# Kernel tuning notes

Measured on AMD Instinct MI355X. Metric: run time of the kernel, lower is better.

Reference implementation:

```python
import jax, jax.numpy as jnp
import numpy as np

N = 100000      # nodes
E = 1600000     # edges (avg degree 16)
D_IN, D_H, D_OUT = 128, 128, 64
NORM_SCALE = 1.0
EPS = 1e-6


def setup_inputs() -> dict:
    key = jax.random.key(0)
    ks = jax.random.split(key, 9)
    x = jax.random.normal(ks[0], (N, D_IN), dtype=jnp.float32)
    edge_index = jax.random.randint(ks[1], (2, E), 0, N, dtype=jnp.int32)
    edge_weight = jax.random.uniform(ks[2], (E,), dtype=jnp.float32)
    # GraphConv = Linear then spmm(adj, .); Glorot-ish init for weights
    W0 = jax.random.normal(ks[3], (D_IN, D_H), dtype=jnp.float32) / np.float32(np.sqrt(D_IN))
    b0 = jnp.zeros((D_H,), jnp.float32)
    W1 = jax.random.normal(ks[4], (D_H, D_H), dtype=jnp.float32) / np.float32(np.sqrt(D_H))
    b1 = jnp.zeros((D_H,), jnp.float32)
    Wout = jax.random.normal(ks[5], (D_H, D_OUT), dtype=jnp.float32) / np.float32(np.sqrt(D_H))
    bout = jnp.zeros((D_OUT,), jnp.float32)
    return {"x": x, "edge_index": edge_index, "edge_weight": edge_weight,
            "W0": W0, "b0": b0, "W1": W1, "b1": b1, "Wout": Wout, "bout": bout}


def _pair_norm(h):
    # PairNorm mode 'PN': center columns, divide by sqrt(mean squared row norm)
    h = h - jnp.mean(h, axis=0, keepdims=True)
    rownorm_mean = jnp.sqrt(EPS + jnp.mean(jnp.sum(h * h, axis=1)))
    return NORM_SCALE * h / rownorm_mean


def reference(x, edge_index, edge_weight, W0, b0, W1, b1, Wout, bout):
    src = edge_index[0]
    dst = edge_index[1]

    def graph_conv(h, W, b):
        h = h @ W + b                              # [N, d_out]
        msg = edge_weight[:, None] * h[src]        # [E, d_out] gather
        return jax.ops.segment_sum(msg, dst, num_segments=N)  # spmm(adj, h)

    x_old = jnp.zeros((), jnp.float32)
    for (W, b) in ((W0, b0), (W1, b1)):
        # dropout p=0 -> identity (omitted)
        h = graph_conv(x, W, b)
        h = jax.nn.relu(_pair_norm(h))
        x = h + x_old        # residual=1 -> skip every layer
        x_old = x
    return graph_conv(x, Wout, bout)
```

## Files before the change

kernel.cpp:

```cpp
#include <hip/hip_runtime.h>

#define N_NODES 100000
#define N_EDGES 1600000
#define DH 128
#define DOUT 64
#define EPS 1e-6f
#define NBINS 8
#define BINW 12500
#define NREP 64

typedef __attribute__((ext_vector_type(8))) short s8v;
typedef __attribute__((ext_vector_type(4))) float f32x4;

__device__ inline unsigned bfround(float f) {
    unsigned u = __float_as_uint(f);
    return (u + 0x7fffu + ((u >> 16) & 1u)) >> 16;
}
__device__ inline unsigned pack2(float a, float b) { return bfround(a) | (bfround(b) << 16); }
__device__ inline float blo(unsigned u) { return __uint_as_float(u << 16); }
__device__ inline float bhi(unsigned u) { return __uint_as_float(u & 0xffff0000u); }

template <int COLS, int PN>
__global__ __launch_bounds__(256) void gemm_mfma(const void* __restrict__ Xav,
                                                 const float* __restrict__ muA,
                                                 const float* __restrict__ invA,
                                                 const unsigned* __restrict__ Xbu2,
                                                 const float* __restrict__ muB,
                                                 const float* __restrict__ invB,
                                                 const float* __restrict__ W,
                                                 const float* __restrict__ bias,
                                                 unsigned* __restrict__ Y, int nrows) {
    constexpr int CT = COLS / 16;
    __shared__ unsigned wtu[COLS][64];
    __shared__ unsigned xbu[64][64];

    const int tid = threadIdx.x;
    const int wv = tid >> 6;
    const int lane = tid & 63;
    const float sA = (PN >= 1) ? invA[0] : 0.f;
    const float sB = (PN == 2) ? invB[0] : 0.f;

    {
        ushort* wts = (ushort*)wtu;
        constexpr int NV4 = 128 * COLS / 4;
        for (int i = tid; i < NV4; i += 256) {
            int k = i / (COLS / 4);
            int c4 = i % (COLS / 4);
            float4 w4 = reinterpret_cast<const float4*>(W)[i];
            float vals[4] = {w4.x, w4.y, w4.z, w4.w};
            int u = k >> 1, kb = k & 1;
#pragma unroll
            for (int j = 0; j < 4; ++j) {
                int c = c4 * 4 + j;
                int us = u ^ ((c & 7) << 2);
                wts[c * 128 + us * 2 + kb] = (ushort)bfround(vals[j]);
            }
        }
    }

    float bv[CT];
#pragma unroll
    for (int f = 0; f < CT; ++f) bv[f] = bias[f * 16 + (lane & 15)];

    const int row0 = blockIdx.x * 128;
    const int myr = (wv << 4) + (lane & 15);

#pragma unroll
    for (int ms = 0; ms < 2; ++ms) {
        const int rb = row0 + ms * 64;
        __syncthreads();
        if constexpr (PN == 0) {
            const float* Xa = (const float*)Xav;
            for (int i = tid; i < 2048; i += 256) {
                int r = i >> 5;
                int c4 = i & 31;
                float4 v = make_float4(0.f, 0.f, 0.f, 0.f);
                if (rb + r < nrows) v = reinterpret_cast<const float4*>(Xa + (size_t)(rb + r) * 128)[c4];
                int sw = (r & 7) << 2;
                xbu[r][(c4 * 2) ^ sw] = pack2(v.x, v.y);
                xbu[r][(c4 * 2 + 1) ^ sw] = pack2(v.z, v.w);
            }
        } else {
            const unsigned* Xa = (const unsigned*)Xav;
            for (int i = tid; i < 1024; i += 256) {
                int r = i >> 4;
                int c4 = i & 15;
                float v0 = 0.f, v1 = 0.f, v2 = 0.f, v3 = 0.f, v4 = 0.f, v5 = 0.f, v6 = 0.f,
                      v7 = 0.f;
                if (rb + r < nrows) {
                    uint4 uv = reinterpret_cast<const uint4*>(Xa + (size_t)(rb + r) * 64)[c4];
                    float4 ma = reinterpret_cast<const float4*>(muA)[c4 * 2];
                    float4 mb = reinterpret_cast<const float4*>(muA)[c4 * 2 + 1];
                    v0 = fmaxf((blo(uv.x) - ma.x) * sA, 0.f);
                    v1 = fmaxf((bhi(uv.x) - ma.y) * sA, 0.f);
                    v2 = fmaxf((blo(uv.y) - ma.z) * sA, 0.f);
                    v3 = fmaxf((bhi(uv.y) - ma.w) * sA, 0.f);
                    v4 = fmaxf((blo(uv.z) - mb.x) * sA, 0.f);
                    v5 = fmaxf((bhi(uv.z) - mb.y) * sA, 0.f);
                    v6 = fmaxf((blo(uv.w) - mb.z) * sA, 0.f);
                    v7 = fmaxf((bhi(uv.w) - mb.w) * sA, 0.f);
                    if constexpr (PN == 2) {
                        uint4 u2 = reinterpret_cast<const uint4*>(Xbu2 + (size_t)(rb + r) * 64)[c4];
                        float4 na = reinterpret_cast<const float4*>(muB)[c4 * 2];
                        float4 nb = reinterpret_cast<const float4*>(muB)[c4 * 2 + 1];
                        v0 += fmaxf((blo(u2.x) - na.x) * sB, 0.f);
                        v1 += fmaxf((bhi(u2.x) - na.y) * sB, 0.f);
                        v2 += fmaxf((blo(u2.y) - na.z) * sB, 0.f);
                        v3 += fmaxf((bhi(u2.y) - na.w) * sB, 0.f);
                        v4 += fmaxf((blo(u2.z) - nb.x) * sB, 0.f);
                        v5 += fmaxf((bhi(u2.z) - nb.y) * sB, 0.f);
                        v6 += fmaxf((blo(u2.w) - nb.z) * sB, 0.f);
                        v7 += fmaxf((bhi(u2.w) - nb.w) * sB, 0.f);
                    }
                }
                int sw = (r & 7) << 2;
                xbu[r][(c4 * 4 + 0) ^ sw] = pack2(v0, v1);
                xbu[r][(c4 * 4 + 1) ^ sw] = pack2(v2, v3);
                xbu[r][(c4 * 4 + 2) ^ sw] = pack2(v4, v5);
                xbu[r][(c4 * 4 + 3) ^ sw] = pack2(v6, v7);
            }
        }
        __syncthreads();

        f32x4 acc[CT];
#pragma unroll
        for (int f = 0; f < CT; ++f) acc[f] = (f32x4){0.f, 0.f, 0.f, 0.f};
        const int xsw = (myr & 7) << 2;
#pragma unroll
        for (int kc = 0; kc < 4; ++kc) {
            const int u0 = kc * 16 + (lane >> 4) * 4;
            s8v a = *reinterpret_cast<const s8v*>(&xbu[myr][u0 ^ xsw]);
#pragma unroll
            for (int f = 0; f < CT; ++f) {
                const int c = f * 16 + (lane & 15);
                s8v b = *reinterpret_cast<const s8v*>(&wtu[c][u0 ^ ((c & 7) << 2)]);
                acc[f] = __builtin_amdgcn_mfma_f32_16x16x32_bf16(a, b, acc[f], 0, 0, 0);
            }
        }

#pragma unroll
        for (int f = 0; f < CT; ++f) {
#pragma unroll
            for (int r = 0; r < 4; ++r) {
                float v = acc[f][r] + bv[f];
                float p = __shfl_xor(v, 1, 64);
                unsigned pk = (lane & 1) ? pack2(p, v) : pack2(v, p);
                int grow = rb + (wv << 4) + ((lane >> 4) << 2) + r;
                if (grow < nrows && ((lane & 1) == (f & 1))) {
                    Y[(size_t)grow * (COLS / 2) + f * 8 + ((lane & 15) >> 1)] = pk;
                }
            }
        }
    }
}

__global__ __launch_bounds__(256) void hist_kernel(const int* __restrict__ dst,
                                                   int* __restrict__ counts) {
    int i = blockIdx.x * blockDim.x + threadIdx.x;
    const int stride = gridDim.x * blockDim.x;
    for (; i < N_EDGES / 4; i += stride) {
        int4 d = reinterpret_cast<const int4*>(dst)[i];
        atomicAdd(&counts[d.x], 1);
        atomicAdd(&counts[d.y], 1);
        atomicAdd(&counts[d.z], 1);
        atomicAdd(&counts[d.w], 1);
    }
}

__global__ __launch_bounds__(1024) void scan_kernel(const int* __restrict__ counts,
                                                    int* __restrict__ rowptr) {
    __shared__ int wsum[16];
    const int tid = threadIdx.x;
    const int lane = tid & 63;
    const int w = tid >> 6;
    int offset = 0;
    if (tid == 0) rowptr[0] = 0;
    for (int base = 0; base < N_NODES; base += 4096) {
        int i = base + tid * 4;
        int4 v = make_int4(0, 0, 0, 0);
        if (i < N_NODES) v = *reinterpret_cast<const int4*>(counts + i);
        int p0 = v.x, p1 = p0 + v.y, p2 = p1 + v.z, p3 = p2 + v.w;
        int incl = p3;
#pragma unroll
        for (int d = 1; d < 64; d <<= 1) {
            int t = __shfl_up(incl, d, 64);
            if (lane >= d) incl += t;
        }
        if (lane == 63) wsum[w] = incl;
        __syncthreads();
        if (w == 0 && lane < 16) {
            int t = wsum[lane];
#pragma unroll
            for (int d = 1; d < 16; d <<= 1) {
                int u = __shfl_up(t, d, 64);
                if (lane >= d) t += u;
            }
            wsum[lane] = t;
        }
        __syncthreads();
        int woff = (w == 0) ? 0 : wsum[w - 1];
        int chunk_total = wsum[15];
        int tbase = offset + woff + incl - p3;
        if (i < N_NODES) {
            rowptr[i + 1] = tbase + p0;
            rowptr[i + 2] = tbase + p1;
            rowptr[i + 3] = tbase + p2;
            rowptr[i + 4] = tbase + p3;
        }
        offset += chunk_total;
        __syncthreads();
    }
}

__global__ __launch_bounds__(256) void bucket_kernel(const int* __restrict__ src,
                                                     const int* __restrict__ dst,
                                                     const float* __restrict__ ew,
                                                     const int* __restrict__ rowptr,
                                                     int* __restrict__ fill,
                                                     int2* __restrict__ em) {
    const int myBin = blockIdx.x & (NBINS - 1);
    const int lo = myBin * BINW;
    const int hi = lo + BINW;
    int e = (blockIdx.x >> 3) * 256 + threadIdx.x;
    const int stride = (gridDim.x >> 3) * 256;
    for (; e < N_EDGES; e += stride) {
        int d = dst[e];
        if (d >= lo && d < hi) {
            int pos = atomicAdd(&fill[d], 1);
            em[rowptr[d] + pos] = make_int2(src[e], __float_as_int(ew[e]));
        }
    }
}

__global__ __launch_bounds__(256) void agg128b_kernel(const unsigned* __restrict__ Hb,
                                                      const int* __restrict__ rowptr,
                                                      const int2* __restrict__ em,
                                                      unsigned* __restrict__ Bb,
                                                      float* __restrict__ cs_part,
                                                      float* __restrict__ ss_part) {
    __shared__ int2 smeta[4][64];
    __shared__ float cs[4][128];
    __shared__ float ssw[4];
    const int wv = threadIdx.x >> 6;
    const int lane = threadIdx.x & 63;
    const int half = lane >> 5;
    const int col2 = lane & 31;
    const int node = blockIdx.x * 4 + wv;
    const int beg = rowptr[node];
    const int end = rowptr[node + 1];
    const int2* sm = smeta[wv];
    float a0 = 0.f, a1 = 0.f, a2 = 0.f, a3 = 0.f;

    for (int c = beg; c < end; c += 64) {
        smeta[wv][lane] = (c + lane < end) ? em[c + lane] : make_int2(0, 0);
        const int cnt = min(64, end - c);
        const int rounds = (cnt + 15) >> 4;
        for (int g = 0; g < rounds; ++g) {
            const int b = g * 16 + half;
            int2 m0 = sm[b + 0];
            int2 m1 = sm[b + 2];
            int2 m2 = sm[b + 4];
            int2 m3 = sm[b + 6];
            int2 m4 = sm[b + 8];
            int2 m5 = sm[b + 10];
            int2 m6 = sm[b + 12];
            int2 m7 = sm[b + 14];
            uint2 u0 = *reinterpret_cast<const uint2*>(Hb + (size_t)m0.x * 64 + col2 * 2);
            uint2 u1 = *reinterpret_cast<const uint2*>(Hb + (size_t)m1.x * 64 + col2 * 2);
            uint2 u2 = *reinterpret_cast<const uint2*>(Hb + (size_t)m2.x * 64 + col2 * 2);
            uint2 u3 = *reinterpret_cast<const uint2*>(Hb + (size_t)m3.x * 64 + col2 * 2);
            uint2 u4 = *reinterpret_cast<const uint2*>(Hb + (size_t)m4.x * 64 + col2 * 2);
            uint2 u5 = *reinterpret_cast<const uint2*>(Hb + (size_t)m5.x * 64 + col2 * 2);
            uint2 u6 = *reinterpret_cast<const uint2*>(Hb + (size_t)m6.x * 64 + col2 * 2);
            uint2 u7 = *reinterpret_cast<const uint2*>(Hb + (size_t)m7.x * 64 + col2 * 2);
            float w0 = __int_as_float(m0.y), w1 = __int_as_float(m1.y);
            float w2 = __int_as_float(m2.y), w3 = __int_as_float(m3.y);
            float w4 = __int_as_float(m4.y), w5 = __int_as_float(m5.y);
            float w6 = __int_as_float(m6.y), w7 = __int_as_float(m7.y);
            a0 += w0 * blo(u0.x); a1 += w0 * bhi(u0.x); a2 += w0 * blo(u0.y); a3 += w0 * bhi(u0.y);
            a0 += w1 * blo(u1.x); a1 += w1 * bhi(u1.x); a2 += w1 * blo(u1.y); a3 += w1 * bhi(u1.y);
            a0 += w2 * blo(u2.x); a1 += w2 * bhi(u2.x); a2 += w2 * blo(u2.y); a3 += w2 * bhi(u2.y);
            a0 += w3 * blo(u3.x); a1 += w3 * bhi(u3.x); a2 += w3 * blo(u3.y); a3 += w3 * bhi(u3.y);
            a0 += w4 * blo(u4.x); a1 += w4 * bhi(u4.x); a2 += w4 * blo(u4.y); a3 += w4 * bhi(u4.y);
            a0 += w5 * blo(u5.x); a1 += w5 * bhi(u5.x); a2 += w5 * blo(u5.y); a3 += w5 * bhi(u5.y);
            a0 += w6 * blo(u6.x); a1 += w6 * bhi(u6.x); a2 += w6 * blo(u6.y); a3 += w6 * bhi(u6.y);
            a0 += w7 * blo(u7.x); a1 += w7 * bhi(u7.x); a2 += w7 * blo(u7.y); a3 += w7 * bhi(u7.y);
        }
    }
    a0 += __shfl_xor(a0, 32, 64);
    a1 += __shfl_xor(a1, 32, 64);
    a2 += __shfl_xor(a2, 32, 64);
    a3 += __shfl_xor(a3, 32, 64);

    float sq = 0.f;
    if (lane < 32) {
        uint2 op;
        op.x = pack2(a0, a1);
        op.y = pack2(a2, a3);
        *reinterpret_cast<uint2*>(Bb + (size_t)node * 64 + col2 * 2) = op;
        cs[wv][col2 * 4 + 0] = a0;
        cs[wv][col2 * 4 + 1] = a1;
        cs[wv][col2 * 4 + 2] = a2;
        cs[wv][col2 * 4 + 3] = a3;
        sq = a0 * a0 + a1 * a1 + a2 * a2 + a3 * a3;
    }
#pragma unroll
    for (int off = 32; off; off >>= 1) sq += __shfl_down(sq, off, 64);
    if (lane == 0) ssw[wv] = sq;
    __syncthreads();
    const int rep = blockIdx.x & (NREP - 1);
    if (threadIdx.x < 128) {
        float s = cs[0][threadIdx.x] + cs[1][threadIdx.x] + cs[2][threadIdx.x] + cs[3][threadIdx.x];
        atomicAdd(&cs_part[rep * 128 + threadIdx.x], s);
    }
    if (threadIdx.x == 0) atomicAdd(&ss_part[rep], ssw[0] + ssw[1] + ssw[2] + ssw[3]);
}

__global__ __launch_bounds__(256) void agg64b_kernel(const unsigned* __restrict__ Hb,
                                                     const int* __restrict__ rowptr,
                                                     const int2* __restrict__ em,
                                                     float* __restrict__ out) {
    __shared__ int2 smeta[4][64];
    const int wv = threadIdx.x >> 6;
    const int lane = threadIdx.x & 63;
    const int q = lane >> 4;
    const int col2 = lane & 15;
    const int node = blockIdx.x * 4 + wv;
    const int beg = rowptr[node];
    const int end = rowptr[node + 1];
    const int2* sm = smeta[wv];
    float a0 = 0.f, a1 = 0.f, a2 = 0.f, a3 = 0.f;

    for (int c = beg; c < end; c += 64) {
        smeta[wv][lane] = (c + lane < end) ? em[c + lane] : make_int2(0, 0);
        const int cnt = min(64, end - c);
        const int rounds = (cnt + 31) >> 5;
        for (int g = 0; g < rounds; ++g) {
            const int b = g * 32 + q;
            int2 m0 = sm[b + 0];
            int2 m1 = sm[b + 4];
            int2 m2 = sm[b + 8];
            int2 m3 = sm[b + 12];
            int2 m4 = sm[b + 16];
            int2 m5 = sm[b + 20];
            int2 m6 = sm[b + 24];
            int2 m7 = sm[b + 28];
            uint2 u0 = *reinterpret_cast<const uint2*>(Hb + (size_t)m0.x * 32 + col2 * 2);
            uint2 u1 = *reinterpret_cast<const uint2*>(Hb + (size_t)m1.x * 32 + col2 * 2);
            uint2 u2 = *reinterpret_cast<const uint2*>(Hb + (size_t)m2.x * 32 + col2 * 2);
            uint2 u3 = *reinterpret_cast<const uint2*>(Hb + (size_t)m3.x * 32 + col2 * 2);
            uint2 u4 = *reinterpret_cast<const uint2*>(Hb + (size_t)m4.x * 32 + col2 * 2);
            uint2 u5 = *reinterpret_cast<const uint2*>(Hb + (size_t)m5.x * 32 + col2 * 2);
            uint2 u6 = *reinterpret_cast<const uint2*>(Hb + (size_t)m6.x * 32 + col2 * 2);
            uint2 u7 = *reinterpret_cast<const uint2*>(Hb + (size_t)m7.x * 32 + col2 * 2);
            float w0 = __int_as_float(m0.y), w1 = __int_as_float(m1.y);
            float w2 = __int_as_float(m2.y), w3 = __int_as_float(m3.y);
            float w4 = __int_as_float(m4.y), w5 = __int_as_float(m5.y);
            float w6 = __int_as_float(m6.y), w7 = __int_as_float(m7.y);
            a0 += w0 * blo(u0.x); a1 += w0 * bhi(u0.x); a2 += w0 * blo(u0.y); a3 += w0 * bhi(u0.y);
            a0 += w1 * blo(u1.x); a1 += w1 * bhi(u1.x); a2 += w1 * blo(u1.y); a3 += w1 * bhi(u1.y);
            a0 += w2 * blo(u2.x); a1 += w2 * bhi(u2.x); a2 += w2 * blo(u2.y); a3 += w2 * bhi(u2.y);
            a0 += w3 * blo(u3.x); a1 += w3 * bhi(u3.x); a2 += w3 * blo(u3.y); a3 += w3 * bhi(u3.y);
            a0 += w4 * blo(u4.x); a1 += w4 * bhi(u4.x); a2 += w4 * blo(u4.y); a3 += w4 * bhi(u4.y);
            a0 += w5 * blo(u5.x); a1 += w5 * bhi(u5.x); a2 += w5 * blo(u5.y); a3 += w5 * bhi(u5.y);
            a0 += w6 * blo(u6.x); a1 += w6 * bhi(u6.x); a2 += w6 * blo(u6.y); a3 += w6 * bhi(u6.y);
            a0 += w7 * blo(u7.x); a1 += w7 * bhi(u7.x); a2 += w7 * blo(u7.y); a3 += w7 * bhi(u7.y);
        }
    }
    a0 += __shfl_xor(a0, 16, 64); a0 += __shfl_xor(a0, 32, 64);
    a1 += __shfl_xor(a1, 16, 64); a1 += __shfl_xor(a1, 32, 64);
    a2 += __shfl_xor(a2, 16, 64); a2 += __shfl_xor(a2, 32, 64);
    a3 += __shfl_xor(a3, 16, 64); a3 += __shfl_xor(a3, 32, 64);
    if (lane < 16) {
        *reinterpret_cast<float4*>(out + (size_t)node * DOUT + col2 * 4) =
            make_float4(a0, a1, a2, a3);
    }
}

__global__ void finalize_stats(const float* __restrict__ cs_part,
                               const float* __restrict__ ss_part, float* __restrict__ mu,
                               float* __restrict__ inv) {
    const int t = threadIdx.x;
    float m = 0.f;
    for (int r = 0; r < NREP; ++r) m += cs_part[r * 128 + t];
    float mean = m / (float)N_NODES;
    mu[t] = mean;
    float v = mean * mean;
    __shared__ float partl[2];
    __shared__ float sstot;
#pragma unroll
    for (int off = 32; off; off >>= 1) v += __shfl_down(v, off, 64);
    if ((t & 63) == 0) partl[t >> 6] = v;
    float ss = (t < NREP) ? ss_part[t] : 0.f;
#pragma unroll
    for (int off = 32; off; off >>= 1) ss += __shfl_down(ss, off, 64);
    if (t == 0) sstot = ss;
    __syncthreads();
    if (t == 0) {
        float musq = partl[0] + partl[1];
        float s = (sstot - (float)N_NODES * musq) / (float)N_NODES;
        inv[0] = rsqrtf(EPS + s);
    }
}

extern "C" void kernel_launch(void* const* d_in, const int* in_sizes, int n_in,
                              void* d_out, int out_size, void* d_ws, size_t ws_size,
                              hipStream_t stream) {
    const float* x = (const float*)d_in[0];
    const int* edge_index = (const int*)d_in[1];
    const float* ew = (const float*)d_in[2];
    const float* W0 = (const float*)d_in[3];
    const float* b0 = (const float*)d_in[4];
    const float* W1 = (const float*)d_in[5];
    const float* b1 = (const float*)d_in[6];
    const float* Wout = (const float*)d_in[7];
    const float* bout = (const float*)d_in[8];

    const int* src = edge_index;
    const int* dst = edge_index + N_EDGES;
    float* out = (float*)d_out;

    unsigned* base = (unsigned*)d_ws;
    unsigned* Hb = base;
    unsigned* B1b = base + (size_t)N_NODES * 64;
    unsigned* B2b = B1b + (size_t)N_NODES * 64;
    int2* em = (int2*)(B2b + (size_t)N_NODES * 64);
    int* counts = (int*)(em + N_EDGES);
    int* fill = counts + N_NODES;
    int* rowptr = fill + N_NODES;
    size_t soff = (size_t)(rowptr + N_NODES + 1 - (int*)base);
    soff = (soff + 3) & ~(size_t)3;
    float* stats = (float*)base + soff;
    float* cs_part1 = stats;
    float* ss_part1 = cs_part1 + NREP * 128;
    float* cs_part2 = ss_part1 + NREP;
    float* ss_part2 = cs_part2 + NREP * 128;
    float* mu1 = ss_part2 + NREP;
    float* inv1 = mu1 + 128;
    float* mu2 = inv1 + 4;
    float* inv2 = mu2 + 128;

    const int gemm_grid = (N_NODES + 127) / 128;
    const int agg_grid = N_NODES / 4;

    hipMemsetAsync(counts, 0, (size_t)2 * N_NODES * sizeof(int), stream);
    hipMemsetAsync(stats, 0, (size_t)2 * (NREP * 128 + NREP) * sizeof(float), stream);

    hist_kernel<<<1024, 256, 0, stream>>>(dst, counts);
    scan_kernel<<<1, 1024, 0, stream>>>(counts, rowptr);
    bucket_kernel<<<2048, 256, 0, stream>>>(src, dst, ew, rowptr, fill, em);

    gemm_mfma<128, 0><<<gemm_grid, 256, 0, stream>>>(
        x, nullptr, nullptr, nullptr, nullptr, nullptr, W0, b0, Hb, N_NODES);
    agg128b_kernel<<<agg_grid, 256, 0, stream>>>(Hb, rowptr, em, B1b, cs_part1, ss_part1);
    finalize_stats<<<1, 128, 0, stream>>>(cs_part1, ss_part1, mu1, inv1);

    gemm_mfma<128, 1><<<gemm_grid, 256, 0, stream>>>(
        B1b, mu1, inv1, nullptr, nullptr, nullptr, W1, b1, Hb, N_NODES);
    agg128b_kernel<<<agg_grid, 256, 0, stream>>>(Hb, rowptr, em, B2b, cs_part2, ss_part2);
    finalize_stats<<<1, 128, 0, stream>>>(cs_part2, ss_part2, mu2, inv2);

    gemm_mfma<64, 2><<<gemm_grid, 256, 0, stream>>>(
        B2b, mu2, inv2, B1b, mu1, inv1, Wout, bout, Hb, N_NODES);
    agg64b_kernel<<<agg_grid, 256, 0, stream>>>(Hb, rowptr, em, out);
}
```

Baseline: 539.4 us.

## Split 128-wide aggregation into column slices across blocks for cache locality

Replaces the per-node full-row aggregation kernel with a column-sliced version. Each block handles one of eight 16-column slices for 16 nodes, and each wave processes 16 edges at a time with 4 lanes per edge. The aim is a smaller working set per concurrent block slice, so gathered rows hit in cache better and more gathers are in flight per wave. In exchange, the edge metadata (em, rowptr) is re-read eight times, each gather is only 16 bytes, and there are more shuffle reductions and atomics.

```diff
diff --git a/kernel.cpp b/kernel.cpp
--- a/kernel.cpp
+++ b/kernel.cpp
@@ -232,88 +232,71 @@
     }
 }
 
-__global__ __launch_bounds__(256) void agg128b_kernel(const unsigned* __restrict__ Hb,
+__global__ __launch_bounds__(256) void agg128s_kernel(const unsigned* __restrict__ Hb,
                                                       const int* __restrict__ rowptr,
                                                       const int2* __restrict__ em,
                                                       unsigned* __restrict__ Bb,
                                                       float* __restrict__ cs_part,
                                                       float* __restrict__ ss_part) {
-    __shared__ int2 smeta[4][64];
-    __shared__ float cs[4][128];
-    __shared__ float ssw[4];
+    const int slice = blockIdx.x & 7;
+    const int grp = blockIdx.x >> 3;
     const int wv = threadIdx.x >> 6;
     const int lane = threadIdx.x & 63;
-    const int half = lane >> 5;
-    const int col2 = lane & 31;
-    const int node = blockIdx.x * 4 + wv;
-    const int beg = rowptr[node];
-    const int end = rowptr[node + 1];
-    const int2* sm = smeta[wv];
-    float a0 = 0.f, a1 = 0.f, a2 = 0.f, a3 = 0.f;
-
-    for (int c = beg; c < end; c += 64) {
-        smeta[wv][lane] = (c + lane < end) ? em[c + lane] : make_int2(0, 0);
-        const int cnt = min(64, end - c);
-        const int rounds = (cnt + 15) >> 4;
-        for (int g = 0; g < rounds; ++g) {
-            const int b = g * 16 + half;
-            int2 m0 = sm[b + 0];
-            int2 m1 = sm[b + 2];
-            int2 m2 = sm[b + 4];
-            int2 m3 = sm[b + 6];
-            int2 m4 = sm[b + 8];
-            int2 m5 = sm[b + 10];
-            int2 m6 = sm[b + 12];
-            int2 m7 = sm[b + 14];
-            uint2 u0 = *reinterpret_cast<const uint2*>(Hb + (size_t)m0.x * 64 + col2 * 2);
-            uint2 u1 = *reinterpret_cast<const uint2*>(Hb + (size_t)m1.x * 64 + col2 * 2);
-            uint2 u2 = *reinterpret_cast<const uint2*>(Hb + (size_t)m2.x * 64 + col2 * 2);
-            uint2 u3 = *reinterpret_cast<const uint2*>(Hb + (size_t)m3.x * 64 + col2 * 2);
-            uint2 u4 = *reinterpret_cast<const uint2*>(Hb + (size_t)m4.x * 64 + col2 * 2);
-            uint2 u5 = *reinterpret_cast<const uint2*>(Hb + (size_t)m5.x * 64 + col2 * 2);
-            uint2 u6 = *reinterpret_cast<const uint2*>(Hb + (size_t)m6.x * 64 + col2 * 2);
-            uint2 u7 = *reinterpret_cast<const uint2*>(Hb + (size_t)m7.x * 64 + col2 * 2);
-            float w0 = __int_as_float(m0.y), w1 = __int_as_float(m1.y);
-            float w2 = __int_as_float(m2.y), w3 = __int_as_float(m3.y);
-            float w4 = __int_as_float(m4.y), w5 = __int_as_float(m5.y);
-            float w6 = __int_as_float(m6.y), w7 = __int_as_float(m7.y);
-            a0 += w0 * blo(u0.x); a1 += w0 * bhi(u0.x); a2 += w0 * blo(u0.y); a3 += w0 * bhi(u0.y);
-            a0 += w1 * blo(u1.x); a1 += w1 * bhi(u1.x); a2 += w1 * blo(u1.y); a3 += w1 * bhi(u1.y);
-            a0 += w2 * blo(u2.x); a1 += w2 * bhi(u2.x); a2 += w2 * blo(u2.y); a3 += w2 * bhi(u2.y);
-            a0 += w3 * blo(u3.x); a1 += w3 * bhi(u3.x); a2 += w3 * blo(u3.y); a3 += w3 * bhi(u3.y);
-            a0 += w4 * blo(u4.x); a1 += w4 * bhi(u4.x); a2 += w4 * blo(u4.y); a3 += w4 * bhi(u4.y);
-            a0 += w5 * blo(u5.x); a1 += w5 * bhi(u5.x); a2 += w5 * blo(u5.y); a3 += w5 * bhi(u5.y);
-            a0 += w6 * blo(u6.x); a1 += w6 * bhi(u6.x); a2 += w6 * blo(u6.y); a3 += w6 * bhi(u6.y);
-            a0 += w7 * blo(u7.x); a1 += w7 * bhi(u7.x); a2 += w7 * blo(u7.y); a3 += w7 * bhi(u7.y);
-        }
-    }
-    a0 += __shfl_xor(a0, 32, 64);
-    a1 += __shfl_xor(a1, 32, 64);
-    a2 += __shfl_xor(a2, 32, 64);
-    a3 += __shfl_xor(a3, 32, 64);
-
-    float sq = 0.f;
-    if (lane < 32) {
-        uint2 op;
-        op.x = pack2(a0, a1);
-        op.y = pack2(a2, a3);
-        *reinterpret_cast<uint2*>(Bb + (size_t)node * 64 + col2 * 2) = op;
-        cs[wv][col2 * 4 + 0] = a0;
-        cs[wv][col2 * 4 + 1] = a1;
-        cs[wv][col2 * 4 + 2] = a2;
-        cs[wv][col2 * 4 + 3] = a3;
-        sq = a0 * a0 + a1 * a1 + a2 * a2 + a3 * a3;
-    }
-#pragma unroll
-    for (int off = 32; off; off >>= 1) sq += __shfl_down(sq, off, 64);
-    if (lane == 0) ssw[wv] = sq;
-    __syncthreads();
-    const int rep = blockIdx.x & (NREP - 1);
-    if (threadIdx.x < 128) {
-        float s = cs[0][threadIdx.x] + cs[1][threadIdx.x] + cs[2][threadIdx.x] + cs[3][threadIdx.x];
-        atomicAdd(&cs_part[rep * 128 + threadIdx.x], s);
-    }
-    if (threadIdx.x == 0) atomicAdd(&ss_part[rep], ssw[0] + ssw[1] + ssw[2] + ssw[3]);
+    const int sub = lane >> 2;
+    const int f = lane & 3;
+    const unsigned* hsl = Hb + slice * 8 + f * 2;
+    const int nbase = grp * 16 + wv * 4;
+
+    float cs0 = 0.f, cs1 = 0.f, cs2 = 0.f, cs3 = 0.f, ssl = 0.f;
+
+#pragma unroll
+    for (int nn = 0; nn < 4; ++nn) {
+        const int node = nbase + nn;
+        const int beg = rowptr[node];
+        const int end = rowptr[node + 1];
+        float a0 = 0.f, a1 = 0.f, a2 = 0.f, a3 = 0.f;
+        for (int c = beg; c < end; c += 16) {
+            const int ei = c + sub;
+            int2 m = (ei < end) ? em[ei] : make_int2(0, 0);
+            uint2 u = *reinterpret_cast<const uint2*>(hsl + (size_t)m.x * 64);
+            float w = __int_as_float(m.y);
+            a0 += w * blo(u.x);
+            a1 += w * bhi(u.x);
+            a2 += w * blo(u.y);
+            a3 += w * bhi(u.y);
+        }
+        a0 += __shfl_xor(a0, 4, 64); a0 += __shfl_xor(a0, 8, 64);
+        a0 += __shfl_xor(a0, 16, 64); a0 += __shfl_xor(a0, 32, 64);
+        a1 += __shfl_xor(a1, 4, 64); a1 += __shfl_xor(a1, 8, 64);
+        a1 += __shfl_xor(a1, 16, 64); a1 += __shfl_xor(a1, 32, 64);
+        a2 += __shfl_xor(a2, 4, 64); a2 += __shfl_xor(a2, 8, 64);
+        a2 += __shfl_xor(a2, 16, 64); a2 += __shfl_xor(a2, 32, 64);
+        a3 += __shfl_xor(a3, 4, 64); a3 += __shfl_xor(a3, 8, 64);
+        a3 += __shfl_xor(a3, 16, 64); a3 += __shfl_xor(a3, 32, 64);
+        if (lane < 4) {
+            uint2 op;
+            op.x = pack2(a0, a1);
+            op.y = pack2(a2, a3);
+            *reinterpret_cast<uint2*>(Bb + (size_t)node * 64 + slice * 8 + lane * 2) = op;
+            cs0 += a0;
+            cs1 += a1;
+            cs2 += a2;
+            cs3 += a3;
+            ssl += a0 * a0 + a1 * a1 + a2 * a2 + a3 * a3;
+        }
+    }
+
+    const int rep = grp & (NREP - 1);
+    if (lane < 4) {
+        float* cp = &cs_part[rep * 128 + slice * 16 + lane * 4];
+        atomicAdd(cp + 0, cs0);
+        atomicAdd(cp + 1, cs1);
+        atomicAdd(cp + 2, cs2);
+        atomicAdd(cp + 3, cs3);
+    }
+    ssl += __shfl_xor(ssl, 1, 64);
+    ssl += __shfl_xor(ssl, 2, 64);
+    if (lane == 0) atomicAdd(&ss_part[rep], ssl);
 }
 
 __global__ __launch_bounds__(256) void agg64b_kernel(const unsigned* __restrict__ Hb,
@@ -441,6 +424,7 @@
     float* inv2 = mu2 + 128;
 
     const int gemm_grid = (N_NODES + 127) / 128;
+    const int aggs_grid = (N_NODES / 16) * 8;
     const int agg_grid = N_NODES / 4;
 
     hipMemsetAsync(counts, 0, (size_t)2 * N_NODES * sizeof(int), stream);
@@ -452,12 +436,12 @@
 
     gemm_mfma<128, 0><<<gemm_grid, 256, 0, stream>>>(
         x, nullptr, nullptr, nullptr, nullptr, nullptr, W0, b0, Hb, N_NODES);
-    agg128b_kernel<<<agg_grid, 256, 0, stream>>>(Hb, rowptr, em, B1b, cs_part1, ss_part1);
+    agg128s_kernel<<<aggs_grid, 256, 0, stream>>>(Hb, rowptr, em, B1b, cs_part1, ss_part1);
     finalize_stats<<<1, 128, 0, stream>>>(cs_part1, ss_part1, mu1, inv1);
 
     gemm_mfma<128, 1><<<gemm_grid, 256, 0, stream>>>(
         B1b, mu1, inv1, nullptr, nullptr, nullptr, W1, b1, Hb, N_NODES);
-    agg128b_kernel<<<agg_grid, 256, 0, stream>>>(Hb, rowptr, em, B2b, cs_part2, ss_part2);
+    agg128s_kernel<<<aggs_grid, 256, 0, stream>>>(Hb, rowptr, em, B2b, cs_part2, ss_part2);
     finalize_stats<<<1, 128, 0, stream>>>(cs_part2, ss_part2, mu2, inv2);
 
     gemm_mfma<64, 2><<<gemm_grid, 256, 0, stream>>>(
```

New measurement: 1.889 ms. 250% more time.
